# Optimization experiments

Measured on AMD Instinct MI355X. Metric: run time of the kernel, lower is better.

Reference implementation:

```python
import jax, jax.numpy as jnp
import numpy as np

N_NODES = 100000
N_EDGES = 1600000
D = 128
N_LAYERS = 3  # GIN num_layers = n_layers + 1 with n_layers = 2
BN_EPS = 1e-5


def _batchnorm(x, gamma, beta):
    # Training-mode BatchNorm1d over the node axis (biased variance, as torch uses
    # for normalization).
    mean = jnp.mean(x, axis=0)
    var = jnp.mean((x - mean) ** 2, axis=0)
    return (x - mean) * jax.lax.rsqrt(var + BN_EPS) * gamma + beta


def setup_inputs() -> dict:
    key = jax.random.key(0)
    ks = jax.random.split(key, 5)
    features = jax.random.normal(ks[0], (N_NODES, D), dtype=jnp.float32)
    W = jax.random.normal(ks[1], (N_LAYERS, D, D), dtype=jnp.float32) * 0.05
    b = jnp.zeros((N_LAYERS, D), dtype=jnp.float32)
    eps = jnp.zeros((N_LAYERS,), dtype=jnp.float32)  # learn_eps init 0
    bn1_gamma = jnp.ones((N_LAYERS, D), dtype=jnp.float32)
    bn1_beta = jnp.zeros((N_LAYERS, D), dtype=jnp.float32)
    bn2_gamma = jnp.ones((N_LAYERS, D), dtype=jnp.float32)
    bn2_beta = jnp.zeros((N_LAYERS, D), dtype=jnp.float32)
    src = jax.random.randint(ks[2], (N_EDGES,), 0, N_NODES, dtype=jnp.int64 if jax.config.jax_enable_x64 else jnp.int32)
    dst = jax.random.randint(ks[3], (N_EDGES,), 0, N_NODES, dtype=jnp.int64 if jax.config.jax_enable_x64 else jnp.int32)
    return {
        'features': features, 'W': W, 'b': b, 'eps': eps,
        'bn1_gamma': bn1_gamma, 'bn1_beta': bn1_beta,
        'bn2_gamma': bn2_gamma, 'bn2_beta': bn2_beta,
        'src': src, 'dst': dst,
    }


def reference(features, W, b, eps, bn1_gamma, bn1_beta, bn2_gamma, bn2_beta, src, dst):
    n = features.shape[0]
    h = features
    hidden_rep = [h]
    for i in range(N_LAYERS):
        # GINConv, 'sum' aggregation: (1+eps)*h_v + sum_{u->v} h_u
        agg = jax.ops.segment_sum(h[src], dst, num_segments=n)
        z = (1.0 + eps[i]) * h + agg
        # ApplyNodeFunc: Linear (num_mlp_layers=1) -> BN -> ReLU
        z = z @ W[i] + b[i]
        z = jax.nn.relu(_batchnorm(z, bn1_gamma[i], bn1_beta[i]))
        # GIN.forward: outer BN -> ReLU
        z = jax.nn.relu(_batchnorm(z, bn2_gamma[i], bn2_beta[i]))
        h = z
        hidden_rep.append(h)
    # torch.stack(hidden_rep) -> [n_layers+2, N, D]
    return jnp.stack(hidden_rep, axis=0)
```

## Files before the change

### kernel.cpp

```cpp
#include <hip/hip_runtime.h>
#include <hip/hip_bf16.h>

#define DD 128

typedef __attribute__((ext_vector_type(8))) short bfrag8;
typedef __attribute__((ext_vector_type(4))) float f32x4;

__device__ __forceinline__ float bf16lo(unsigned int u) {
    union { unsigned int i; float f; } c; c.i = u << 16; return c.f;
}
__device__ __forceinline__ float bf16hi(unsigned int u) {
    union { unsigned int i; float f; } c; c.i = u & 0xffff0000u; return c.f;
}
__device__ __forceinline__ unsigned short f2bf(float f) {
    union { float f; unsigned int i; } c; c.f = f;
    unsigned int x = c.i;
    unsigned int r = (x + 0x7fffu + ((x >> 16) & 1u)) >> 16;
    return (unsigned short)r;
}

__global__ void k_setup(const int* __restrict__ dst, int* __restrict__ deg, int E,
                        const float* __restrict__ features, float* __restrict__ out0,
                        unsigned int* __restrict__ hb, int total4,
                        const float* __restrict__ W, unsigned short* __restrict__ Wt) {
    int gtid = blockIdx.x * blockDim.x + threadIdx.x;
    int gsz = gridDim.x * blockDim.x;
    for (int i = gtid; i < E; i += gsz) atomicAdd(&deg[dst[i]], 1);
    for (int i = gtid; i < total4; i += gsz) {
        float4 v = ((const float4*)features)[i];
        ((float4*)out0)[i] = v;
        unsigned int lo = (unsigned int)f2bf(v.x) | ((unsigned int)f2bf(v.y) << 16);
        unsigned int hi = (unsigned int)f2bf(v.z) | ((unsigned int)f2bf(v.w) << 16);
        ((uint2*)hb)[i] = make_uint2(lo, hi);
    }
    for (int i = gtid; i < 3 * 128 * 128; i += gsz) {
        int l = i >> 14, r = i & 16383, k = r >> 7, n = r & 127;
        Wt[(l << 14) + n * 128 + k] = f2bf(W[i]);
    }
}

__global__ void k_scan1(const int* __restrict__ deg, int* __restrict__ partials, int Nn) {
    __shared__ int sm[256];
    int tid = threadIdx.x;
    int base = (blockIdx.x << 10) + 4 * tid;
    int s = 0;
    if (base + 3 < Nn) {
        int4 v = *(const int4*)&deg[base];
        s = v.x + v.y + v.z + v.w;
    } else {
        for (int j = 0; j < 4; j++) if (base + j < Nn) s += deg[base + j];
    }
    sm[tid] = s;
    __syncthreads();
    for (int off = 128; off > 0; off >>= 1) {
        if (tid < off) sm[tid] += sm[tid + off];
        __syncthreads();
    }
    if (tid == 0) partials[blockIdx.x] = sm[0];
}

__global__ void k_scan3(const int* __restrict__ deg, const int* __restrict__ partials,
                        int* __restrict__ row_start, int Nn, int E, int nchunk) {
    __shared__ int sp[256];
    __shared__ int sm[256];
    int tid = threadIdx.x, c = blockIdx.x;
    int p = (tid < nchunk) ? partials[tid] : 0;
    sp[tid] = p;
    __syncthreads();
    for (int off = 1; off < 256; off <<= 1) {
        int t = (tid >= off) ? sp[tid - off] : 0;
        __syncthreads();
        sp[tid] += t;
        __syncthreads();
    }
    int chunkpref = (c == 0) ? 0 : sp[c - 1];

    int base = (c << 10) + 4 * tid;
    int d0 = 0, d1 = 0, d2 = 0, d3 = 0;
    if (base + 3 < Nn) {
        int4 v = *(const int4*)&deg[base];
        d0 = v.x; d1 = v.y; d2 = v.z; d3 = v.w;
    } else {
        if (base + 0 < Nn) d0 = deg[base + 0];
        if (base + 1 < Nn) d1 = deg[base + 1];
        if (base + 2 < Nn) d2 = deg[base + 2];
        if (base + 3 < Nn) d3 = deg[base + 3];
    }
    int ts = d0 + d1 + d2 + d3;
    sm[tid] = ts;
    __syncthreads();
    for (int off = 1; off < 256; off <<= 1) {
        int t = (tid >= off) ? sm[tid - off] : 0;
        __syncthreads();
        sm[tid] += t;
        __syncthreads();
    }
    int run = chunkpref + sm[tid] - ts;
    if (base + 0 < Nn) row_start[base + 0] = run; run += d0;
    if (base + 1 < Nn) row_start[base + 1] = run; run += d1;
    if (base + 2 < Nn) row_start[base + 2] = run; run += d2;
    if (base + 3 < Nn) row_start[base + 3] = run;
    if (c == 0 && tid == 0) row_start[Nn] = E;
}

__global__ void k_scatter(const int* __restrict__ src, const int* __restrict__ dst,
                          const int* __restrict__ row_start, int* __restrict__ cursor,
                          int* __restrict__ csr, int E) {
    int i = blockIdx.x * blockDim.x + threadIdx.x;
    if (i < E) {
        int d = dst[i];
        int pos = row_start[d] + atomicAdd(&cursor[d], 1);
        csr[pos] = src[i];
    }
}

__global__ void k_gather(const unsigned int* __restrict__ hb, const int* __restrict__ row_start,
                         const int* __restrict__ csr, const float* __restrict__ eps, int layer,
                         unsigned int* __restrict__ zb, int Nn) {
    int wv = threadIdx.x >> 6, lane = threadIdx.x & 63;
    int v = blockIdx.x * 4 + wv;
    if (v >= Nn) return;
    float e1 = 1.0f + eps[layer];
    unsigned int hs = hb[(size_t)v * 64 + lane];
    float ax = e1 * bf16lo(hs);
    float ay = e1 * bf16hi(hs);
    int beg = row_start[v], end = row_start[v + 1];
    int e = beg;
    for (; e + 7 < end; e += 8) {
        int u0 = csr[e], u1 = csr[e + 1], u2 = csr[e + 2], u3 = csr[e + 3];
        int u4 = csr[e + 4], u5 = csr[e + 5], u6 = csr[e + 6], u7 = csr[e + 7];
        unsigned int h0 = hb[(size_t)u0 * 64 + lane];
        unsigned int h1 = hb[(size_t)u1 * 64 + lane];
        unsigned int h2 = hb[(size_t)u2 * 64 + lane];
        unsigned int h3 = hb[(size_t)u3 * 64 + lane];
        unsigned int h4 = hb[(size_t)u4 * 64 + lane];
        unsigned int h5 = hb[(size_t)u5 * 64 + lane];
        unsigned int h6 = hb[(size_t)u6 * 64 + lane];
        unsigned int h7 = hb[(size_t)u7 * 64 + lane];
        ax += bf16lo(h0) + bf16lo(h1) + bf16lo(h2) + bf16lo(h3)
            + bf16lo(h4) + bf16lo(h5) + bf16lo(h6) + bf16lo(h7);
        ay += bf16hi(h0) + bf16hi(h1) + bf16hi(h2) + bf16hi(h3)
            + bf16hi(h4) + bf16hi(h5) + bf16hi(h6) + bf16hi(h7);
    }
    for (; e < end; e++) {
        unsigned int hu = hb[(size_t)csr[e] * 64 + lane];
        ax += bf16lo(hu); ay += bf16hi(hu);
    }
    zb[(size_t)v * 64 + lane] = (unsigned int)f2bf(ax) | ((unsigned int)f2bf(ay) << 16);
}

__launch_bounds__(256)
__global__ void k_gemm(const unsigned short* __restrict__ zb, const unsigned short* __restrict__ Wt,
                       const float* __restrict__ bias, int layer, float* __restrict__ y,
                       float* __restrict__ stl, int Nn) {
    __shared__ unsigned short Al[64 * 136];
    __shared__ unsigned short Bl[128 * 136];
    int tid = threadIdx.x;
    int m0 = blockIdx.x * 64;
    const unsigned short* Wl = Wt + (layer << 14);
    #pragma unroll
    for (int p = 0; p < 8; p++) {
        int slot = p * 256 + tid;
        int n = slot >> 4, c = slot & 15;
        *(uint4*)&Bl[n * 136 + c * 8] = *(const uint4*)&Wl[n * 128 + c * 8];
    }
    #pragma unroll
    for (int p = 0; p < 4; p++) {
        int slot = p * 256 + tid;
        int r = slot >> 4, c = slot & 15;
        int grow = m0 + r;
        uint4 val = make_uint4(0, 0, 0, 0);
        if (grow < Nn) val = *(const uint4*)&zb[(size_t)grow * 128 + c * 8];
        *(uint4*)&Al[r * 136 + c * 8] = val;
    }
    __syncthreads();

    int lane = tid & 63, wv = tid >> 6;
    int tcol = lane & 15, quad = lane >> 4;
    f32x4 acc[4][2];
    #pragma unroll
    for (int a = 0; a < 4; a++)
        #pragma unroll
        for (int b2 = 0; b2 < 2; b2++) acc[a][b2] = (f32x4){0.f, 0.f, 0.f, 0.f};

    #pragma unroll
    for (int kk = 0; kk < 128; kk += 32) {
        int kb = kk + quad * 8;
        bfrag8 af[4], bf[2];
        #pragma unroll
        for (int mt = 0; mt < 4; mt++)
            af[mt] = *(const bfrag8*)&Al[(16 * mt + tcol) * 136 + kb];
        #pragma unroll
        for (int nt = 0; nt < 2; nt++)
            bf[nt] = *(const bfrag8*)&Bl[(32 * wv + 16 * nt + tcol) * 136 + kb];
        #pragma unroll
        for (int mt = 0; mt < 4; mt++)
            #pragma unroll
            for (int nt = 0; nt < 2; nt++)
                acc[mt][nt] = __builtin_amdgcn_mfma_f32_16x16x32_bf16(af[mt], bf[nt], acc[mt][nt], 0, 0, 0);
    }

    #pragma unroll
    for (int nt = 0; nt < 2; nt++) {
        int col = 32 * wv + 16 * nt + tcol;
        float bcol = bias[layer * 128 + col];
        float psum = 0.f, psq = 0.f;
        #pragma unroll
        for (int mt = 0; mt < 4; mt++) {
            #pragma unroll
            for (int r = 0; r < 4; r++) {
                int row = m0 + 16 * mt + quad * 4 + r;
                float val = acc[mt][nt][r] + bcol;
                if (row < Nn) {
                    y[(size_t)row * 128 + col] = val;
                    psum += val;
                    psq += val * val;
                }
            }
        }
        psum += __shfl_xor(psum, 16); psq += __shfl_xor(psq, 16);
        psum += __shfl_xor(psum, 32); psq += __shfl_xor(psq, 32);
        if (lane < 16) {
            atomicAdd(&stl[col], psum);
            atomicAdd(&stl[128 + col], psq);
        }
    }
}

__launch_bounds__(256)
__global__ void k_stats2(const float* __restrict__ y, float* __restrict__ stl,
                         const float* __restrict__ g1, const float* __restrict__ b1,
                         int layer, int total4, float invN) {
    __shared__ float red[512];
    int tid = threadIdx.x;
    if (tid < 128) {
        float m = stl[tid] * invN;
        float var = stl[128 + tid] * invN - m * m;
        float rstd = rsqrtf(var + 1e-5f);
        float s = g1[layer * 128 + tid] * rstd;
        red[tid] = s;
        red[128 + tid] = b1[layer * 128 + tid] - m * s;
        red[256 + tid] = 0.f;
        red[384 + tid] = 0.f;
    }
    __syncthreads();
    int lane = tid & 63;
    int cbase = (4 * tid) & 127;
    float s1r[4], sh1r[4];
    #pragma unroll
    for (int j = 0; j < 4; j++) { s1r[j] = red[cbase + j]; sh1r[j] = red[128 + cbase + j]; }
    float ps[4] = {0.f, 0.f, 0.f, 0.f}, pq[4] = {0.f, 0.f, 0.f, 0.f};
    int gtid = blockIdx.x * 256 + tid;
    int gsz = gridDim.x * 256;
    for (int i = gtid; i < total4; i += gsz) {
        float4 v = ((const float4*)y)[i];
        float t0 = fmaxf(v.x * s1r[0] + sh1r[0], 0.f);
        float t1 = fmaxf(v.y * s1r[1] + sh1r[1], 0.f);
        float t2 = fmaxf(v.z * s1r[2] + sh1r[2], 0.f);
        float t3 = fmaxf(v.w * s1r[3] + sh1r[3], 0.f);
        ps[0] += t0; pq[0] += t0 * t0;
        ps[1] += t1; pq[1] += t1 * t1;
        ps[2] += t2; pq[2] += t2 * t2;
        ps[3] += t3; pq[3] += t3 * t3;
    }
    #pragma unroll
    for (int j = 0; j < 4; j++) {
        ps[j] += __shfl_xor(ps[j], 32);
        pq[j] += __shfl_xor(pq[j], 32);
    }
    if (lane < 32) {
        #pragma unroll
        for (int j = 0; j < 4; j++) {
            atomicAdd(&red[256 + cbase + j], ps[j]);
            atomicAdd(&red[384 + cbase + j], pq[j]);
        }
    }
    __syncthreads();
    if (tid < 128) {
        atomicAdd(&stl[256 + tid], red[256 + tid]);
        atomicAdd(&stl[384 + tid], red[384 + tid]);
    }
}

__launch_bounds__(256)
__global__ void k_apply(const float* __restrict__ y, const float* __restrict__ stl,
                        const float* __restrict__ g1, const float* __restrict__ b1,
                        const float* __restrict__ g2, const float* __restrict__ b2,
                        int layer, float* __restrict__ outl, unsigned int* __restrict__ hb,
                        int total4, float invN) {
    __shared__ float red[512];
    int tid = threadIdx.x;
    if (tid < 128) {
        float m1 = stl[tid] * invN;
        float v1 = stl[128 + tid] * invN - m1 * m1;
        float r1 = rsqrtf(v1 + 1e-5f);
        float s1 = g1[layer * 128 + tid] * r1;
        red[tid] = s1;
        red[128 + tid] = b1[layer * 128 + tid] - m1 * s1;
        float m2 = stl[256 + tid] * invN;
        float v2 = stl[384 + tid] * invN - m2 * m2;
        float r2 = rsqrtf(v2 + 1e-5f);
        float s2 = g2[layer * 128 + tid] * r2;
        red[256 + tid] = s2;
        red[384 + tid] = b2[layer * 128 + tid] - m2 * s2;
    }
    __syncthreads();
    int cbase = (4 * tid) & 127;
    float s1a[4], sh1a[4], s2a[4], sh2a[4];
    #pragma unroll
    for (int j = 0; j < 4; j++) {
        s1a[j]  = red[cbase + j];       sh1a[j] = red[128 + cbase + j];
        s2a[j]  = red[256 + cbase + j]; sh2a[j] = red[384 + cbase + j];
    }
    int gtid = blockIdx.x * 256 + tid;
    int gsz = gridDim.x * 256;
    for (int i = gtid; i < total4; i += gsz) {
        float4 v = ((const float4*)y)[i];
        float t0 = fmaxf(v.x * s1a[0] + sh1a[0], 0.f);
        float t1 = fmaxf(v.y * s1a[1] + sh1a[1], 0.f);
        float t2 = fmaxf(v.z * s1a[2] + sh1a[2], 0.f);
        float t3 = fmaxf(v.w * s1a[3] + sh1a[3], 0.f);
        float o0 = fmaxf(t0 * s2a[0] + sh2a[0], 0.f);
        float o1 = fmaxf(t1 * s2a[1] + sh2a[1], 0.f);
        float o2 = fmaxf(t2 * s2a[2] + sh2a[2], 0.f);
        float o3 = fmaxf(t3 * s2a[3] + sh2a[3], 0.f);
        ((float4*)outl)[i] = make_float4(o0, o1, o2, o3);
        unsigned int lo = (unsigned int)f2bf(o0) | ((unsigned int)f2bf(o1) << 16);
        unsigned int hi = (unsigned int)f2bf(o2) | ((unsigned int)f2bf(o3) << 16);
        ((uint2*)hb)[i] = make_uint2(lo, hi);
    }
}

extern "C" void kernel_launch(void* const* d_in, const int* in_sizes, int n_in,
                              void* d_out, int out_size, void* d_ws, size_t ws_size,
                              hipStream_t stream) {
    const float* features = (const float*)d_in[0];
    const float* W        = (const float*)d_in[1];
    const float* bias     = (const float*)d_in[2];
    const float* eps      = (const float*)d_in[3];
    const float* g1       = (const float*)d_in[4];
    const float* b1       = (const float*)d_in[5];
    const float* g2       = (const float*)d_in[6];
    const float* b2       = (const float*)d_in[7];
    const int*   src      = (const int*)d_in[8];
    const int*   dst      = (const int*)d_in[9];

    const int Nn = in_sizes[0] / DD;
    const int E  = in_sizes[8];
    float* out = (float*)d_out;

    char* w = (char*)d_ws;
    auto alloc = [&](size_t bytes) -> char* {
        char* p = w;
        w += (bytes + 255) & ~(size_t)255;
        return p;
    };
    int*   deg    = (int*)alloc((size_t)Nn * 4);
    int*   cursor = (int*)alloc((size_t)Nn * 4);
    float* stats  = (float*)alloc(3 * 512 * 4);
    char*  zero_end = w;
    int* row_start = (int*)alloc((size_t)(Nn + 1) * 4);
    int* partials  = (int*)alloc(1024);
    int* csr       = (int*)alloc((size_t)E * 4);
    unsigned int* hb = (unsigned int*)alloc((size_t)Nn * 64 * 4);
    unsigned int* zb = (unsigned int*)alloc((size_t)Nn * 64 * 4);
    unsigned short* Wt = (unsigned short*)alloc((size_t)3 * 128 * 128 * 2);
    float* yb = (float*)alloc((size_t)Nn * 128 * 4);

    const int total4 = Nn * DD / 4;
    const float invN = 1.0f / (float)Nn;
    const int nchunk = (Nn + 1023) / 1024;

    hipMemsetAsync(deg, 0, (size_t)(zero_end - (char*)deg), stream);

    k_setup<<<(E + 255) / 256, 256, 0, stream>>>(dst, deg, E, features, out, hb, total4, W, Wt);
    k_scan1<<<nchunk, 256, 0, stream>>>(deg, partials, Nn);
    k_scan3<<<nchunk, 256, 0, stream>>>(deg, partials, row_start, Nn, E, nchunk);
    k_scatter<<<(E + 255) / 256, 256, 0, stream>>>(src, dst, row_start, cursor, csr, E);

    for (int l = 0; l < 3; l++) {
        float* stl = stats + l * 512;
        float* outl = out + (size_t)(l + 1) * Nn * DD;
        k_gather<<<(Nn + 3) / 4, 256, 0, stream>>>(hb, row_start, csr, eps, l, zb, Nn);
        k_gemm<<<(Nn + 63) / 64, 256, 0, stream>>>((const unsigned short*)zb, Wt, bias, l, yb,
                                                   stl, Nn);
        k_stats2<<<512, 256, 0, stream>>>(yb, stl, g1, b1, l, total4, invN);
        k_apply<<<1024, 256, 0, stream>>>(yb, stl, g1, b1, g2, b2, l, outl, hb, total4, invN);
    }
}
```

Before: 857.7 us.

## Fuse neighbor gather into GEMM and store pre-BN activations as bf16

Merges the gather kernel into the GEMM kernel so aggregated rows go straight into shared memory. This removes the zb round trip through global memory and one launch per layer. W fragments are now read directly from global memory instead of being staged in LDS, and the intermediate y buffer is stored as bf16, so the stats and apply kernels read half as many bytes using 8-wide vector loads. The trade-offs are fewer concurrent gather waves per block (each wave serially handles 16 nodes), uncached global reads of W in the MFMA loop, and extra rounding of pre-BN values to bf16.

```diff
diff --git a/kernel.cpp b/kernel.cpp
--- a/kernel.cpp
+++ b/kernel.cpp
@@ -11,6 +11,9 @@
 }
 __device__ __forceinline__ float bf16hi(unsigned int u) {
     union { unsigned int i; float f; } c; c.i = u & 0xffff0000u; return c.f;
+}
+__device__ __forceinline__ float bf16f(unsigned short u) {
+    union { unsigned int i; float f; } c; c.i = ((unsigned int)u) << 16; return c.f;
 }
 __device__ __forceinline__ unsigned short f2bf(float f) {
     union { float f; unsigned int i; } c; c.f = f;
@@ -114,69 +117,55 @@
     }
 }
 
-__global__ void k_gather(const unsigned int* __restrict__ hb, const int* __restrict__ row_start,
-                         const int* __restrict__ csr, const float* __restrict__ eps, int layer,
-                         unsigned int* __restrict__ zb, int Nn) {
-    int wv = threadIdx.x >> 6, lane = threadIdx.x & 63;
-    int v = blockIdx.x * 4 + wv;
-    if (v >= Nn) return;
-    float e1 = 1.0f + eps[layer];
-    unsigned int hs = hb[(size_t)v * 64 + lane];
-    float ax = e1 * bf16lo(hs);
-    float ay = e1 * bf16hi(hs);
-    int beg = row_start[v], end = row_start[v + 1];
-    int e = beg;
-    for (; e + 7 < end; e += 8) {
-        int u0 = csr[e], u1 = csr[e + 1], u2 = csr[e + 2], u3 = csr[e + 3];
-        int u4 = csr[e + 4], u5 = csr[e + 5], u6 = csr[e + 6], u7 = csr[e + 7];
-        unsigned int h0 = hb[(size_t)u0 * 64 + lane];
-        unsigned int h1 = hb[(size_t)u1 * 64 + lane];
-        unsigned int h2 = hb[(size_t)u2 * 64 + lane];
-        unsigned int h3 = hb[(size_t)u3 * 64 + lane];
-        unsigned int h4 = hb[(size_t)u4 * 64 + lane];
-        unsigned int h5 = hb[(size_t)u5 * 64 + lane];
-        unsigned int h6 = hb[(size_t)u6 * 64 + lane];
-        unsigned int h7 = hb[(size_t)u7 * 64 + lane];
-        ax += bf16lo(h0) + bf16lo(h1) + bf16lo(h2) + bf16lo(h3)
-            + bf16lo(h4) + bf16lo(h5) + bf16lo(h6) + bf16lo(h7);
-        ay += bf16hi(h0) + bf16hi(h1) + bf16hi(h2) + bf16hi(h3)
-            + bf16hi(h4) + bf16hi(h5) + bf16hi(h6) + bf16hi(h7);
-    }
-    for (; e < end; e++) {
-        unsigned int hu = hb[(size_t)csr[e] * 64 + lane];
-        ax += bf16lo(hu); ay += bf16hi(hu);
-    }
-    zb[(size_t)v * 64 + lane] = (unsigned int)f2bf(ax) | ((unsigned int)f2bf(ay) << 16);
-}
-
 __launch_bounds__(256)
-__global__ void k_gemm(const unsigned short* __restrict__ zb, const unsigned short* __restrict__ Wt,
-                       const float* __restrict__ bias, int layer, float* __restrict__ y,
-                       float* __restrict__ stl, int Nn) {
+__global__ void k_gg(const unsigned int* __restrict__ hb, const int* __restrict__ row_start,
+                     const int* __restrict__ csr, const float* __restrict__ eps, int layer,
+                     const unsigned short* __restrict__ Wt, const float* __restrict__ bias,
+                     unsigned short* __restrict__ yb, float* __restrict__ stl, int Nn) {
     __shared__ unsigned short Al[64 * 136];
-    __shared__ unsigned short Bl[128 * 136];
     int tid = threadIdx.x;
     int m0 = blockIdx.x * 64;
+    int wv = tid >> 6, lane = tid & 63;
+
+    float e1 = 1.0f + eps[layer];
+    for (int r8 = 0; r8 < 16; r8++) {
+        int r = (wv << 4) + r8;
+        int v = m0 + r;
+        unsigned int packed = 0;
+        if (v < Nn) {
+            unsigned int hs = hb[(size_t)v * 64 + lane];
+            float ax = e1 * bf16lo(hs);
+            float ay = e1 * bf16hi(hs);
+            int beg = row_start[v], end = row_start[v + 1];
+            int e = beg;
+            for (; e + 7 < end; e += 8) {
+                int u0 = csr[e], u1 = csr[e + 1], u2 = csr[e + 2], u3 = csr[e + 3];
+                int u4 = csr[e + 4], u5 = csr[e + 5], u6 = csr[e + 6], u7 = csr[e + 7];
+                unsigned int h0 = hb[(size_t)u0 * 64 + lane];
+                unsigned int h1 = hb[(size_t)u1 * 64 + lane];
+                unsigned int h2 = hb[(size_t)u2 * 64 + lane];
+                unsigned int h3 = hb[(size_t)u3 * 64 + lane];
+                unsigned int h4 = hb[(size_t)u4 * 64 + lane];
+                unsigned int h5 = hb[(size_t)u5 * 64 + lane];
+                unsigned int h6 = hb[(size_t)u6 * 64 + lane];
+                unsigned int h7 = hb[(size_t)u7 * 64 + lane];
+                ax += bf16lo(h0) + bf16lo(h1) + bf16lo(h2) + bf16lo(h3)
+                    + bf16lo(h4) + bf16lo(h5) + bf16lo(h6) + bf16lo(h7);
+                ay += bf16hi(h0) + bf16hi(h1) + bf16hi(h2) + bf16hi(h3)
+                    + bf16hi(h4) + bf16hi(h5) + bf16hi(h6) + bf16hi(h7);
+            }
+            for (; e < end; e++) {
+                unsigned int hu = hb[(size_t)csr[e] * 64 + lane];
+                ax += bf16lo(hu); ay += bf16hi(hu);
+            }
+            packed = (unsigned int)f2bf(ax) | ((unsigned int)f2bf(ay) << 16);
+        }
+        *(unsigned int*)&Al[r * 136 + 2 * lane] = packed;
+    }
+    __syncthreads();
+
+    int tcol = lane & 15, quad = lane >> 4;
     const unsigned short* Wl = Wt + (layer << 14);
-    #pragma unroll
-    for (int p = 0; p < 8; p++) {
-        int slot = p * 256 + tid;
-        int n = slot >> 4, c = slot & 15;
-        *(uint4*)&Bl[n * 136 + c * 8] = *(const uint4*)&Wl[n * 128 + c * 8];
-    }
-    #pragma unroll
-    for (int p = 0; p < 4; p++) {
-        int slot = p * 256 + tid;
-        int r = slot >> 4, c = slot & 15;
-        int grow = m0 + r;
-        uint4 val = make_uint4(0, 0, 0, 0);
-        if (grow < Nn) val = *(const uint4*)&zb[(size_t)grow * 128 + c * 8];
-        *(uint4*)&Al[r * 136 + c * 8] = val;
-    }
-    __syncthreads();
-
-    int lane = tid & 63, wv = tid >> 6;
-    int tcol = lane & 15, quad = lane >> 4;
     f32x4 acc[4][2];
     #pragma unroll
     for (int a = 0; a < 4; a++)
@@ -192,7 +181,7 @@
             af[mt] = *(const bfrag8*)&Al[(16 * mt + tcol) * 136 + kb];
         #pragma unroll
         for (int nt = 0; nt < 2; nt++)
-            bf[nt] = *(const bfrag8*)&Bl[(32 * wv + 16 * nt + tcol) * 136 + kb];
+            bf[nt] = *(const bfrag8*)&Wl[(32 * wv + 16 * nt + tcol) * 128 + kb];
         #pragma unroll
         for (int mt = 0; mt < 4; mt++)
             #pragma unroll
@@ -210,11 +199,12 @@
             #pragma unroll
             for (int r = 0; r < 4; r++) {
                 int row = m0 + 16 * mt + quad * 4 + r;
-                float val = acc[mt][nt][r] + bcol;
                 if (row < Nn) {
-                    y[(size_t)row * 128 + col] = val;
-                    psum += val;
-                    psq += val * val;
+                    unsigned short u = f2bf(acc[mt][nt][r] + bcol);
+                    yb[(size_t)row * 128 + col] = u;
+                    float vr = bf16f(u);
+                    psum += vr;
+                    psq += vr * vr;
                 }
             }
         }
@@ -228,9 +218,9 @@
 }
 
 __launch_bounds__(256)
-__global__ void k_stats2(const float* __restrict__ y, float* __restrict__ stl,
+__global__ void k_stats2(const unsigned short* __restrict__ yb, float* __restrict__ stl,
                          const float* __restrict__ g1, const float* __restrict__ b1,
-                         int layer, int total4, float invN) {
+                         int layer, int totalU8, float invN) {
     __shared__ float red[512];
     int tid = threadIdx.x;
     if (tid < 128) {
@@ -245,32 +235,39 @@
     }
     __syncthreads();
     int lane = tid & 63;
-    int cbase = (4 * tid) & 127;
-    float s1r[4], sh1r[4];
-    #pragma unroll
-    for (int j = 0; j < 4; j++) { s1r[j] = red[cbase + j]; sh1r[j] = red[128 + cbase + j]; }
-    float ps[4] = {0.f, 0.f, 0.f, 0.f}, pq[4] = {0.f, 0.f, 0.f, 0.f};
+    int cbase = (8 * tid) & 127;
+    float s1r[8], sh1r[8];
+    #pragma unroll
+    for (int j = 0; j < 8; j++) { s1r[j] = red[cbase + j]; sh1r[j] = red[128 + cbase + j]; }
+    float ps[8], pq[8];
+    #pragma unroll
+    for (int j = 0; j < 8; j++) { ps[j] = 0.f; pq[j] = 0.f; }
     int gtid = blockIdx.x * 256 + tid;
     int gsz = gridDim.x * 256;
-    for (int i = gtid; i < total4; i += gsz) {
-        float4 v = ((const float4*)y)[i];
-        float t0 = fmaxf(v.x * s1r[0] + sh1r[0], 0.f);
-        float t1 = fmaxf(v.y * s1r[1] + sh1r[1], 0.f);
-        float t2 = fmaxf(v.z * s1r[2] + sh1r[2], 0.f);
-        float t3 = fmaxf(v.w * s1r[3] + sh1r[3], 0.f);
-        ps[0] += t0; pq[0] += t0 * t0;
-        ps[1] += t1; pq[1] += t1 * t1;
-        ps[2] += t2; pq[2] += t2 * t2;
-        ps[3] += t3; pq[3] += t3 * t3;
-    }
-    #pragma unroll
-    for (int j = 0; j < 4; j++) {
+    const uint4* yb4 = (const uint4*)yb;
+    for (int i = gtid; i < totalU8; i += gsz) {
+        uint4 v = yb4[i];
+        float f[8];
+        f[0] = bf16lo(v.x); f[1] = bf16hi(v.x);
+        f[2] = bf16lo(v.y); f[3] = bf16hi(v.y);
+        f[4] = bf16lo(v.z); f[5] = bf16hi(v.z);
+        f[6] = bf16lo(v.w); f[7] = bf16hi(v.w);
+        #pragma unroll
+        for (int j = 0; j < 8; j++) {
+            float t = fmaxf(f[j] * s1r[j] + sh1r[j], 0.f);
+            ps[j] += t; pq[j] += t * t;
+        }
+    }
+    #pragma unroll
+    for (int j = 0; j < 8; j++) {
+        ps[j] += __shfl_xor(ps[j], 16);
+        pq[j] += __shfl_xor(pq[j], 16);
         ps[j] += __shfl_xor(ps[j], 32);
         pq[j] += __shfl_xor(pq[j], 32);
     }
-    if (lane < 32) {
-        #pragma unroll
-        for (int j = 0; j < 4; j++) {
+    if (lane < 16) {
+        #pragma unroll
+        for (int j = 0; j < 8; j++) {
             atomicAdd(&red[256 + cbase + j], ps[j]);
             atomicAdd(&red[384 + cbase + j], pq[j]);
         }
@@ -283,11 +280,11 @@
 }
 
 __launch_bounds__(256)
-__global__ void k_apply(const float* __restrict__ y, const float* __restrict__ stl,
+__global__ void k_apply(const unsigned short* __restrict__ yb, const float* __restrict__ stl,
                         const float* __restrict__ g1, const float* __restrict__ b1,
                         const float* __restrict__ g2, const float* __restrict__ b2,
                         int layer, float* __restrict__ outl, unsigned int* __restrict__ hb,
-                        int total4, float invN) {
+                        int totalU8, float invN) {
     __shared__ float red[512];
     int tid = threadIdx.x;
     if (tid < 128) {
@@ -305,29 +302,37 @@
         red[384 + tid] = b2[layer * 128 + tid] - m2 * s2;
     }
     __syncthreads();
-    int cbase = (4 * tid) & 127;
-    float s1a[4], sh1a[4], s2a[4], sh2a[4];
-    #pragma unroll
-    for (int j = 0; j < 4; j++) {
+    int cbase = (8 * tid) & 127;
+    float s1a[8], sh1a[8], s2a[8], sh2a[8];
+    #pragma unroll
+    for (int j = 0; j < 8; j++) {
         s1a[j]  = red[cbase + j];       sh1a[j] = red[128 + cbase + j];
         s2a[j]  = red[256 + cbase + j]; sh2a[j] = red[384 + cbase + j];
     }
     int gtid = blockIdx.x * 256 + tid;
     int gsz = gridDim.x * 256;
-    for (int i = gtid; i < total4; i += gsz) {
-        float4 v = ((const float4*)y)[i];
-        float t0 = fmaxf(v.x * s1a[0] + sh1a[0], 0.f);
-        float t1 = fmaxf(v.y * s1a[1] + sh1a[1], 0.f);
-        float t2 = fmaxf(v.z * s1a[2] + sh1a[2], 0.f);
-        float t3 = fmaxf(v.w * s1a[3] + sh1a[3], 0.f);
-        float o0 = fmaxf(t0 * s2a[0] + sh2a[0], 0.f);
-        float o1 = fmaxf(t1 * s2a[1] + sh2a[1], 0.f);
-        float o2 = fmaxf(t2 * s2a[2] + sh2a[2], 0.f);
-        float o3 = fmaxf(t3 * s2a[3] + sh2a[3], 0.f);
-        ((float4*)outl)[i] = make_float4(o0, o1, o2, o3);
-        unsigned int lo = (unsigned int)f2bf(o0) | ((unsigned int)f2bf(o1) << 16);
-        unsigned int hi = (unsigned int)f2bf(o2) | ((unsigned int)f2bf(o3) << 16);
-        ((uint2*)hb)[i] = make_uint2(lo, hi);
+    const uint4* yb4 = (const uint4*)yb;
+    for (int i = gtid; i < totalU8; i += gsz) {
+        uint4 v = yb4[i];
+        float f[8];
+        f[0] = bf16lo(v.x); f[1] = bf16hi(v.x);
+        f[2] = bf16lo(v.y); f[3] = bf16hi(v.y);
+        f[4] = bf16lo(v.z); f[5] = bf16hi(v.z);
+        f[6] = bf16lo(v.w); f[7] = bf16hi(v.w);
+        float o[8];
+        #pragma unroll
+        for (int j = 0; j < 8; j++) {
+            float t = fmaxf(f[j] * s1a[j] + sh1a[j], 0.f);
+            o[j] = fmaxf(t * s2a[j] + sh2a[j], 0.f);
+        }
+        ((float4*)outl)[2 * i]     = make_float4(o[0], o[1], o[2], o[3]);
+        ((float4*)outl)[2 * i + 1] = make_float4(o[4], o[5], o[6], o[7]);
+        uint4 hbv;
+        hbv.x = (unsigned int)f2bf(o[0]) | ((unsigned int)f2bf(o[1]) << 16);
+        hbv.y = (unsigned int)f2bf(o[2]) | ((unsigned int)f2bf(o[3]) << 16);
+        hbv.z = (unsigned int)f2bf(o[4]) | ((unsigned int)f2bf(o[5]) << 16);
+        hbv.w = (unsigned int)f2bf(o[6]) | ((unsigned int)f2bf(o[7]) << 16);
+        ((uint4*)hb)[i] = hbv;
     }
 }
 
@@ -363,11 +368,11 @@
     int* partials  = (int*)alloc(1024);
     int* csr       = (int*)alloc((size_t)E * 4);
     unsigned int* hb = (unsigned int*)alloc((size_t)Nn * 64 * 4);
-    unsigned int* zb = (unsigned int*)alloc((size_t)Nn * 64 * 4);
     unsigned short* Wt = (unsigned short*)alloc((size_t)3 * 128 * 128 * 2);
-    float* yb = (float*)alloc((size_t)Nn * 128 * 4);
+    unsigned short* yb = (unsigned short*)alloc((size_t)Nn * 128 * 2);
 
     const int total4 = Nn * DD / 4;
+    const int totalU8 = Nn * DD / 8;
     const float invN = 1.0f / (float)Nn;
     const int nchunk = (Nn + 1023) / 1024;
 
@@ -381,10 +386,8 @@
     for (int l = 0; l < 3; l++) {
         float* stl = stats + l * 512;
         float* outl = out + (size_t)(l + 1) * Nn * DD;
-        k_gather<<<(Nn + 3) / 4, 256, 0, stream>>>(hb, row_start, csr, eps, l, zb, Nn);
-        k_gemm<<<(Nn + 63) / 64, 256, 0, stream>>>((const unsigned short*)zb, Wt, bias, l, yb,
-                                                   stl, Nn);
-        k_stats2<<<512, 256, 0, stream>>>(yb, stl, g1, b1, l, total4, invN);
-        k_apply<<<1024, 256, 0, stream>>>(yb, stl, g1, b1, g2, b2, l, outl, hb, total4, invN);
-    }
-}
+        k_gg<<<(Nn + 63) / 64, 256, 0, stream>>>(hb, row_start, csr, eps, l, Wt, bias, yb, stl, Nn);
+        k_stats2<<<512, 256, 0, stream>>>(yb, stl, g1, b1, l, totalU8, invN);
+        k_apply<<<1024, 256, 0, stream>>>(yb, stl, g1, b1, g2, b2, l, outl, hb, totalU8, invN);
+    }
+}
```

Measured after the change: 955.4 us. 1.11x slower.
